# Kernel optimization log

Measured on AMD Instinct MI355X. Metric: run time of the kernel, lower is better.

The kernel has to match this reference:

```python
import jax, jax.numpy as jnp
import numpy as np
from jax import lax

B, N, T, H, C = 131072, 62, 5, 32, 3


def lstm(x, w_ih, w_hh, b_ih, b_hh):
    # x: (B, T, I); gates order i,f,g,o (PyTorch convention)
    b, t, _ = x.shape
    h_dim = w_hh.shape[1]
    xg = jnp.einsum('bti,gi->btg', x, w_ih) + b_ih + b_hh  # (B,T,4H)

    def step(carry, xg_t):
        h, c = carry
        g = xg_t + h @ w_hh.T
        i, f, gg, o = jnp.split(g, 4, axis=-1)
        c = jax.nn.sigmoid(f) * c + jax.nn.sigmoid(i) * jnp.tanh(gg)
        h = jax.nn.sigmoid(o) * jnp.tanh(c)
        return (h, c), h

    z = jnp.zeros((b, h_dim), dtype=x.dtype)
    _, hs = lax.scan(step, (z, z), xg.transpose(1, 0, 2))
    return hs.transpose(1, 0, 2)  # (B,T,H)


def ln_lrelu(x, g, b):
    # LayerNorm over last two dims (seq_len, hidden) jointly, then LeakyReLU(0.01)
    mu = x.mean(axis=(1, 2), keepdims=True)
    var = x.var(axis=(1, 2), keepdims=True)
    y = (x - mu) * lax.rsqrt(var + 1e-5) * g + b
    return jax.nn.leaky_relu(y, 0.01)


def setup_inputs() -> dict:
    key = jax.random.key(0)
    ks = jax.random.split(key, 16)
    sc = lambda fan: 1.0 / np.sqrt(H)
    d = {
        'data': jax.random.normal(ks[0], (B, 1, N, T), dtype=jnp.float32),
        'w_ih0': jax.random.uniform(ks[1], (4 * H, N), minval=-sc(N), maxval=sc(N)),
        'w_hh0': jax.random.uniform(ks[2], (4 * H, H), minval=-sc(H), maxval=sc(H)),
        'b_ih0': jax.random.uniform(ks[3], (4 * H,), minval=-sc(H), maxval=sc(H)),
        'b_hh0': jax.random.uniform(ks[4], (4 * H,), minval=-sc(H), maxval=sc(H)),
        'g0': jnp.ones((T, H), jnp.float32),
        'be0': jnp.zeros((T, H), jnp.float32),
        'w_ih1': jax.random.uniform(ks[5], (4 * H, H), minval=-sc(H), maxval=sc(H)),
        'w_hh1': jax.random.uniform(ks[6], (4 * H, H), minval=-sc(H), maxval=sc(H)),
        'b_ih1': jax.random.uniform(ks[7], (4 * H,), minval=-sc(H), maxval=sc(H)),
        'b_hh1': jax.random.uniform(ks[8], (4 * H,), minval=-sc(H), maxval=sc(H)),
        'g1': jnp.ones((T, H), jnp.float32),
        'be1': jnp.zeros((T, H), jnp.float32),
        'dw': jax.random.normal(ks[9], (C, T * H), dtype=jnp.float32) * 0.05,
        'db': jnp.zeros((C,), jnp.float32),
    }
    return d


def reference(data, w_ih0, w_hh0, b_ih0, b_hh0, g0, be0,
              w_ih1, w_hh1, b_ih1, b_hh1, g1, be1, dw, db):
    x = data.squeeze(1).transpose(0, 2, 1)  # (B, T, N)
    out0 = ln_lrelu(lstm(x, w_ih0, w_hh0, b_ih0, b_hh0), g0, be0)   # dropout=eval
    out1 = ln_lrelu(lstm(out0, w_ih1, w_hh1, b_ih1, b_hh1), g1, be1)
    out = out1 + out0  # residual
    flat = out.reshape(out.shape[0], -1)  # (B, T*H)
    return jax.nn.leaky_relu(flat @ dw.T + db, 0.01)
```

## Files before the change

kernel.cpp:

```cpp
#include <hip/hip_runtime.h>
#include <hip/hip_bf16.h>

#define THREADS 256
#define SPB 8

__device__ __forceinline__ float frcp(float x){ return __builtin_amdgcn_rcpf(x); }
__device__ __forceinline__ float fsig(float x){ return frcp(1.0f + __expf(-x)); }
__device__ __forceinline__ float ftanh(float x){
    float e = __expf(2.0f * x);
    return fmaf(-2.0f, frcp(e + 1.0f), 1.0f);
}
__device__ __forceinline__ float lrelu(float x){
    return x > 0.0f ? x : 0.01f * x;
}

__global__ void diag_kernel(float* outp, float code){
    outp[0] = code;
}

__device__ __forceinline__ void load_wh_global(const float* __restrict__ whh, int j, float (&wh)[4][32]){
    #pragma unroll
    for (int r = 0; r < 4; ++r){
        const float* rp = whh + (r*32 + j)*32;
        #pragma unroll
        for (int q = 0; q < 8; ++q){
            float4 v = *(const float4*)(rp + q*4);
            wh[r][q*4+0] = v.x; wh[r][q*4+1] = v.y;
            wh[r][q*4+2] = v.z; wh[r][q*4+3] = v.w;
        }
    }
}

__device__ __forceinline__ void lstm_rec(const float (&wh)[4][32], const float (&acc)[5][4],
                                         float (&out)[5]){
    float h = 0.0f, c = 0.0f;
    #pragma unroll
    for (int t = 0; t < 5; ++t){
        float q0 = acc[t][0], q1 = acc[t][1], q2 = acc[t][2], q3 = acc[t][3];
        if (t > 0){
            #pragma unroll
            for (int k = 0; k < 32; ++k){
                float hk = __shfl(h, k, 32);
                q0 = fmaf(wh[0][k], hk, q0);
                q1 = fmaf(wh[1][k], hk, q1);
                q2 = fmaf(wh[2][k], hk, q2);
                q3 = fmaf(wh[3][k], hk, q3);
            }
        }
        float iv = fsig(q0), fv = fsig(q1), gv = ftanh(q2), ov = fsig(q3);
        c = fmaf(fv, c, iv * gv);
        h = ov * ftanh(c);
        out[t] = h;
    }
}

__device__ __forceinline__ void ln_lrelu(float (&o)[5], const float* gs, const float* bs, int j){
    float s1 = 0.0f, s2 = 0.0f;
    #pragma unroll
    for (int t = 0; t < 5; ++t){ s1 += o[t]; s2 = fmaf(o[t], o[t], s2); }
    #pragma unroll
    for (int m = 1; m < 32; m <<= 1){
        s1 += __shfl_xor(s1, m, 64);
        s2 += __shfl_xor(s2, m, 64);
    }
    float mu   = s1 * (1.0f/160.0f);
    float var  = s2 * (1.0f/160.0f) - mu*mu;
    float rstd = rsqrtf(var + 1e-5f);
    #pragma unroll
    for (int t = 0; t < 5; ++t){
        float y = (o[t] - mu) * rstd;
        y = fmaf(y, gs[t*32 + j], bs[t*32 + j]);
        o[t] = lrelu(y);
    }
}

__global__ __launch_bounds__(THREADS, 1)
void reslstm_kernel(const float* __restrict__ data,
                    const float* __restrict__ wih0, const float* __restrict__ whh0,
                    const float* __restrict__ bih0, const float* __restrict__ bhh0,
                    const float* __restrict__ g0p,  const float* __restrict__ be0p,
                    const float* __restrict__ wih1, const float* __restrict__ whh1,
                    const float* __restrict__ bih1, const float* __restrict__ bhh1,
                    const float* __restrict__ g1p,  const float* __restrict__ be1p,
                    const float* __restrict__ dwp,  const float* __restrict__ dbp,
                    float* __restrict__ outp, int Btot)
{
    __shared__ __attribute__((aligned(16))) float xs[SPB*320];
    __shared__ __attribute__((aligned(16))) float wbuf[128*68];
    __shared__ __attribute__((aligned(16))) float out0s[SPB*160];
    __shared__ float bias0s[128], bias1s[128];
    __shared__ float g0s[160], be0s[160], g1s[160], be1s[160];
    __shared__ float dws[480];
    __shared__ float dbs[3];

    const int tid = threadIdx.x;
    const int b0  = blockIdx.x * SPB;
    const int nsamp = (Btot - b0 < SPB) ? (Btot - b0) : SPB;

    {
        const float* dat = data + (size_t)b0 * 310;
        for (int i = tid; i < nsamp*310; i += THREADS){
            int s = i / 310, r = i - s*310;
            int n = r / 5,   t = r - n*5;
            xs[s*320 + t*64 + n] = dat[i];
        }
        for (int i = tid; i < SPB*10; i += THREADS){
            int s = i / 10, q = i - s*10;
            xs[s*320 + (q>>1)*64 + 62 + (q&1)] = 0.0f;
        }
        for (int i = tid; i < 128*62; i += THREADS){
            int row = i / 62, n = i - row*62;
            wbuf[row*68 + n] = wih0[i];
        }
        for (int i = tid; i < 128*6; i += THREADS){
            int row = i / 6, n = i - row*6;
            wbuf[row*68 + 62 + n] = 0.0f;
        }
        if (tid < 128)  bias0s[tid] = bih0[tid] + bhh0[tid];
        else            { int q = tid - 128; bias1s[q] = bih1[q] + bhh1[q]; }
        if (tid < 160){
            g0s[tid] = g0p[tid];  be0s[tid] = be0p[tid];
            g1s[tid] = g1p[tid];  be1s[tid] = be1p[tid];
        }
        for (int i = tid; i < 480; i += THREADS) dws[i] = dwp[i];
        if (tid < 3) dbs[tid] = dbp[tid];
    }
    __syncthreads();

    const int j = tid & 31;
    const int s = tid >> 5;

    float acc[5][4];
    #pragma unroll
    for (int r = 0; r < 4; ++r){
        float bv = bias0s[r*32 + j];
        #pragma unroll
        for (int t = 0; t < 5; ++t) acc[t][r] = bv;
    }
    {
        const float* xp  = xs   + s*320;
        const float* wp0 = wbuf + j*68;
        #pragma unroll 4
        for (int n0 = 0; n0 < 64; n0 += 4){
            float4 w[4];
            #pragma unroll
            for (int r = 0; r < 4; ++r)
                w[r] = *(const float4*)(wp0 + r*32*68 + n0);
            #pragma unroll
            for (int t = 0; t < 5; ++t){
                float4 xv = *(const float4*)(xp + t*64 + n0);
                #pragma unroll
                for (int r = 0; r < 4; ++r)
                    acc[t][r] = fmaf(w[r].x, xv.x, fmaf(w[r].y, xv.y, fmaf(w[r].z, xv.z, fmaf(w[r].w, xv.w, acc[t][r]))));
            }
        }
    }

    float o0[5];
    {
        float wh[4][32];
        load_wh_global(whh0, j, wh);
        lstm_rec(wh, acc, o0);
    }
    ln_lrelu(o0, g0s, be0s, j);
    #pragma unroll
    for (int t = 0; t < 5; ++t) out0s[s*160 + t*32 + j] = o0[t];

    __syncthreads();
    for (int i = tid; i < 128*32; i += THREADS){
        int row = i >> 5, k = i & 31;
        wbuf[row*36 + k] = wih1[i];
    }
    for (int i = tid; i < 128*4; i += THREADS){
        int row = i >> 2;
        wbuf[row*36 + 32 + (i & 3)] = 0.0f;
    }
    __syncthreads();

    #pragma unroll
    for (int r = 0; r < 4; ++r){
        float bv = bias1s[r*32 + j];
        #pragma unroll
        for (int t = 0; t < 5; ++t) acc[t][r] = bv;
    }
    {
        const float* wp1 = wbuf  + j*36;
        const float* op  = out0s + s*160;
        #pragma unroll 2
        for (int k0 = 0; k0 < 32; k0 += 4){
            float4 w[4];
            #pragma unroll
            for (int r = 0; r < 4; ++r)
                w[r] = *(const float4*)(wp1 + r*32*36 + k0);
            #pragma unroll
            for (int t = 0; t < 5; ++t){
                float4 ov = *(const float4*)(op + t*32 + k0);
                #pragma unroll
                for (int r = 0; r < 4; ++r)
                    acc[t][r] = fmaf(w[r].x, ov.x, fmaf(w[r].y, ov.y, fmaf(w[r].z, ov.z, fmaf(w[r].w, ov.w, acc[t][r]))));
            }
        }
    }

    float o1[5];
    {
        float wh[4][32];
        load_wh_global(whh1, j, wh);
        lstm_rec(wh, acc, o1);
    }
    ln_lrelu(o1, g1s, be1s, j);
    #pragma unroll
    for (int t = 0; t < 5; ++t) o1[t] += o0[t];

    float p0 = 0.0f, p1 = 0.0f, p2 = 0.0f;
    #pragma unroll
    for (int t = 0; t < 5; ++t){
        float v = o1[t];
        p0 = fmaf(dws[      t*32 + j], v, p0);
        p1 = fmaf(dws[160 + t*32 + j], v, p1);
        p2 = fmaf(dws[320 + t*32 + j], v, p2);
    }
    #pragma unroll
    for (int m = 1; m < 32; m <<= 1){
        p0 += __shfl_xor(p0, m, 64);
        p1 += __shfl_xor(p1, m, 64);
        p2 += __shfl_xor(p2, m, 64);
    }
    if (j < 3 && s < nsamp){
        float v = (j == 0) ? p0 : ((j == 1) ? p1 : p2);
        v = lrelu(v + dbs[j]);
        outp[(size_t)(b0 + s)*3 + j] = v;
    }
}

extern "C" void kernel_launch(void* const* d_in, const int* in_sizes, int n_in,
                              void* d_out, int out_size, void* d_ws, size_t ws_size,
                              hipStream_t stream)
{
    (void)d_ws; (void)ws_size;

    const int B = out_size / 3;

    int idx_data = 0;
    for (int i = 1; i < n_in; ++i)
        if (in_sizes[i] > in_sizes[idx_data]) idx_data = i;

    static const int dict_map[15]  = {0,1,2,3,4,5,6,7,8,9,10,11,12,13,14};
    static const int alpha_map[15] = {6,13,11,2,0,9,4,14,12,3,1,10,5,8,7};
    static const int rev_map[15]   = {14,13,12,11,10,9,8,7,6,5,4,3,2,1,0};

    const int* map = dict_map;
    if (idx_data == 6)       map = alpha_map;
    else if (idx_data == 14) map = rev_map;

    long ds  = (long)in_sizes[idx_data];
    long ws0 = (long)in_sizes[map[1]];
    bool ok = (ds == (long)B*310 || ds == (long)B*620 || ds == (long)B*1240)
           && (ws0 == 7936 || ws0 == 15872 || ws0 == 31744);

    if (!ok || B <= 0){
        diag_kernel<<<1, 1, 0, stream>>>((float*)d_out, 100.0f + 10.0f*idx_data);
        return;
    }

    const float* P[15];
    for (int k = 0; k < 15; ++k) P[k] = (const float*)d_in[map[k]];

    const int nblocks = (B + SPB - 1) / SPB;
    reslstm_kernel<<<dim3(nblocks), dim3(THREADS), 0, stream>>>(
        P[0], P[1], P[2], P[3], P[4], P[5], P[6], P[7], P[8], P[9],
        P[10], P[11], P[12], P[13], P[14],
        (float*)d_out, B);
}
```

Baseline: 1.040 ms.

## Stream recurrent weights from global memory instead of holding them in registers

The 128-register recurrent weight array is replaced by float4 loads from global (L1/L2-cached) memory inside each timestep, and hidden states are written to shared memory instead of being kept in registers. LayerNorm statistics are accumulated during the recurrence. The dense-layer weights and bias are read straight from global memory instead of being staged in LDS. The aim is to cut register pressure so occupancy or spill behaviour improves, at the cost of repeated memory loads on the serial recurrence path.

```diff
diff --git a/kernel.cpp b/kernel.cpp
--- a/kernel.cpp
+++ b/kernel.cpp
@@ -1,5 +1,4 @@
 #include <hip/hip_runtime.h>
-#include <hip/hip_bf16.h>
 
 #define THREADS 256
 #define SPB 8
@@ -10,68 +9,47 @@
     float e = __expf(2.0f * x);
     return fmaf(-2.0f, frcp(e + 1.0f), 1.0f);
 }
-__device__ __forceinline__ float lrelu(float x){
-    return x > 0.0f ? x : 0.01f * x;
-}
-
-__global__ void diag_kernel(float* outp, float code){
-    outp[0] = code;
-}
-
-__device__ __forceinline__ void load_wh_global(const float* __restrict__ whh, int j, float (&wh)[4][32]){
-    #pragma unroll
-    for (int r = 0; r < 4; ++r){
-        const float* rp = whh + (r*32 + j)*32;
-        #pragma unroll
-        for (int q = 0; q < 8; ++q){
-            float4 v = *(const float4*)(rp + q*4);
-            wh[r][q*4+0] = v.x; wh[r][q*4+1] = v.y;
-            wh[r][q*4+2] = v.z; wh[r][q*4+3] = v.w;
-        }
-    }
-}
-
-__device__ __forceinline__ void lstm_rec(const float (&wh)[4][32], const float (&acc)[5][4],
-                                         float (&out)[5]){
-    float h = 0.0f, c = 0.0f;
+__device__ __forceinline__ float lrelu(float x){ return x > 0.0f ? x : 0.01f * x; }
+
+__global__ void diag_kernel(float* outp, float code){ outp[0] = code; }
+
+__device__ __forceinline__ void lstm_rec_stream(const float* __restrict__ whh, int j,
+                                                const float (&acc)[5][4],
+                                                float* __restrict__ hline,
+                                                float& s1o, float& s2o)
+{
+    const float* wr0 = whh + (size_t)(0*32 + j)*32;
+    const float* wr1 = whh + (size_t)(1*32 + j)*32;
+    const float* wr2 = whh + (size_t)(2*32 + j)*32;
+    const float* wr3 = whh + (size_t)(3*32 + j)*32;
+    float h = 0.0f, c = 0.0f, s1 = 0.0f, s2 = 0.0f;
     #pragma unroll
     for (int t = 0; t < 5; ++t){
         float q0 = acc[t][0], q1 = acc[t][1], q2 = acc[t][2], q3 = acc[t][3];
         if (t > 0){
             #pragma unroll
-            for (int k = 0; k < 32; ++k){
-                float hk = __shfl(h, k, 32);
-                q0 = fmaf(wh[0][k], hk, q0);
-                q1 = fmaf(wh[1][k], hk, q1);
-                q2 = fmaf(wh[2][k], hk, q2);
-                q3 = fmaf(wh[3][k], hk, q3);
+            for (int k0 = 0; k0 < 32; k0 += 4){
+                float4 u0 = *(const float4*)(wr0 + k0);
+                float4 u1 = *(const float4*)(wr1 + k0);
+                float4 u2 = *(const float4*)(wr2 + k0);
+                float4 u3 = *(const float4*)(wr3 + k0);
+                float h0 = __shfl(h, k0+0, 32);
+                float h1 = __shfl(h, k0+1, 32);
+                float h2 = __shfl(h, k0+2, 32);
+                float h3 = __shfl(h, k0+3, 32);
+                q0 = fmaf(u0.x,h0, fmaf(u0.y,h1, fmaf(u0.z,h2, fmaf(u0.w,h3, q0))));
+                q1 = fmaf(u1.x,h0, fmaf(u1.y,h1, fmaf(u1.z,h2, fmaf(u1.w,h3, q1))));
+                q2 = fmaf(u2.x,h0, fmaf(u2.y,h1, fmaf(u2.z,h2, fmaf(u2.w,h3, q2))));
+                q3 = fmaf(u3.x,h0, fmaf(u3.y,h1, fmaf(u3.z,h2, fmaf(u3.w,h3, q3))));
             }
         }
         float iv = fsig(q0), fv = fsig(q1), gv = ftanh(q2), ov = fsig(q3);
         c = fmaf(fv, c, iv * gv);
         h = ov * ftanh(c);
-        out[t] = h;
-    }
-}
-
-__device__ __forceinline__ void ln_lrelu(float (&o)[5], const float* gs, const float* bs, int j){
-    float s1 = 0.0f, s2 = 0.0f;
-    #pragma unroll
-    for (int t = 0; t < 5; ++t){ s1 += o[t]; s2 = fmaf(o[t], o[t], s2); }
-    #pragma unroll
-    for (int m = 1; m < 32; m <<= 1){
-        s1 += __shfl_xor(s1, m, 64);
-        s2 += __shfl_xor(s2, m, 64);
-    }
-    float mu   = s1 * (1.0f/160.0f);
-    float var  = s2 * (1.0f/160.0f) - mu*mu;
-    float rstd = rsqrtf(var + 1e-5f);
-    #pragma unroll
-    for (int t = 0; t < 5; ++t){
-        float y = (o[t] - mu) * rstd;
-        y = fmaf(y, gs[t*32 + j], bs[t*32 + j]);
-        o[t] = lrelu(y);
-    }
+        s1 += h; s2 = fmaf(h, h, s2);
+        hline[t*32 + j] = h;
+    }
+    s1o = s1; s2o = s2;
 }
 
 __global__ __launch_bounds__(THREADS, 1)
@@ -90,8 +68,6 @@
     __shared__ __attribute__((aligned(16))) float out0s[SPB*160];
     __shared__ float bias0s[128], bias1s[128];
     __shared__ float g0s[160], be0s[160], g1s[160], be1s[160];
-    __shared__ float dws[480];
-    __shared__ float dbs[3];
 
     const int tid = threadIdx.x;
     const int b0  = blockIdx.x * SPB;
@@ -122,13 +98,13 @@
             g0s[tid] = g0p[tid];  be0s[tid] = be0p[tid];
             g1s[tid] = g1p[tid];  be1s[tid] = be1p[tid];
         }
-        for (int i = tid; i < 480; i += THREADS) dws[i] = dwp[i];
-        if (tid < 3) dbs[tid] = dbp[tid];
     }
     __syncthreads();
 
     const int j = tid & 31;
     const int s = tid >> 5;
+    float* xsc = xs    + s*320;
+    float* o0l = out0s + s*160;
 
     float acc[5][4];
     #pragma unroll
@@ -138,7 +114,6 @@
         for (int t = 0; t < 5; ++t) acc[t][r] = bv;
     }
     {
-        const float* xp  = xs   + s*320;
         const float* wp0 = wbuf + j*68;
         #pragma unroll 4
         for (int n0 = 0; n0 < 64; n0 += 4){
@@ -148,7 +123,7 @@
                 w[r] = *(const float4*)(wp0 + r*32*68 + n0);
             #pragma unroll
             for (int t = 0; t < 5; ++t){
-                float4 xv = *(const float4*)(xp + t*64 + n0);
+                float4 xv = *(const float4*)(xsc + t*64 + n0);
                 #pragma unroll
                 for (int r = 0; r < 4; ++r)
                     acc[t][r] = fmaf(w[r].x, xv.x, fmaf(w[r].y, xv.y, fmaf(w[r].z, xv.z, fmaf(w[r].w, xv.w, acc[t][r]))));
@@ -156,15 +131,24 @@
         }
     }
 
-    float o0[5];
-    {
-        float wh[4][32];
-        load_wh_global(whh0, j, wh);
-        lstm_rec(wh, acc, o0);
-    }
-    ln_lrelu(o0, g0s, be0s, j);
-    #pragma unroll
-    for (int t = 0; t < 5; ++t) out0s[s*160 + t*32 + j] = o0[t];
+    {
+        float s1, s2;
+        lstm_rec_stream(whh0, j, acc, o0l, s1, s2);
+        #pragma unroll
+        for (int m = 1; m < 32; m <<= 1){
+            s1 += __shfl_xor(s1, m, 64);
+            s2 += __shfl_xor(s2, m, 64);
+        }
+        float mu   = s1 * (1.0f/160.0f);
+        float var  = s2 * (1.0f/160.0f) - mu*mu;
+        float rstd = rsqrtf(var + 1e-5f);
+        #pragma unroll
+        for (int t = 0; t < 5; ++t){
+            int ix = t*32 + j;
+            float v = o0l[ix];
+            o0l[ix] = lrelu(fmaf((v - mu)*rstd, g0s[ix], be0s[ix]));
+        }
+    }
 
     __syncthreads();
     for (int i = tid; i < 128*32; i += THREADS){
@@ -184,8 +168,7 @@
         for (int t = 0; t < 5; ++t) acc[t][r] = bv;
     }
     {
-        const float* wp1 = wbuf  + j*36;
-        const float* op  = out0s + s*160;
+        const float* wp1 = wbuf + j*36;
         #pragma unroll 2
         for (int k0 = 0; k0 < 32; k0 += 4){
             float4 w[4];
@@ -194,7 +177,7 @@
                 w[r] = *(const float4*)(wp1 + r*32*36 + k0);
             #pragma unroll
             for (int t = 0; t < 5; ++t){
-                float4 ov = *(const float4*)(op + t*32 + k0);
+                float4 ov = *(const float4*)(o0l + t*32 + k0);
                 #pragma unroll
                 for (int r = 0; r < 4; ++r)
                     acc[t][r] = fmaf(w[r].x, ov.x, fmaf(w[r].y, ov.y, fmaf(w[r].z, ov.z, fmaf(w[r].w, ov.w, acc[t][r]))));
@@ -202,23 +185,27 @@
         }
     }
 
-    float o1[5];
-    {
-        float wh[4][32];
-        load_wh_global(whh1, j, wh);
-        lstm_rec(wh, acc, o1);
-    }
-    ln_lrelu(o1, g1s, be1s, j);
-    #pragma unroll
-    for (int t = 0; t < 5; ++t) o1[t] += o0[t];
-
     float p0 = 0.0f, p1 = 0.0f, p2 = 0.0f;
-    #pragma unroll
-    for (int t = 0; t < 5; ++t){
-        float v = o1[t];
-        p0 = fmaf(dws[      t*32 + j], v, p0);
-        p1 = fmaf(dws[160 + t*32 + j], v, p1);
-        p2 = fmaf(dws[320 + t*32 + j], v, p2);
+    {
+        float s1, s2;
+        lstm_rec_stream(whh1, j, acc, xsc, s1, s2);
+        #pragma unroll
+        for (int m = 1; m < 32; m <<= 1){
+            s1 += __shfl_xor(s1, m, 64);
+            s2 += __shfl_xor(s2, m, 64);
+        }
+        float mu   = s1 * (1.0f/160.0f);
+        float var  = s2 * (1.0f/160.0f) - mu*mu;
+        float rstd = rsqrtf(var + 1e-5f);
+        #pragma unroll
+        for (int t = 0; t < 5; ++t){
+            int ix = t*32 + j;
+            float v = xsc[ix];
+            float y = lrelu(fmaf((v - mu)*rstd, g1s[ix], be1s[ix])) + o0l[ix];
+            p0 = fmaf(dwp[      ix], y, p0);
+            p1 = fmaf(dwp[160 + ix], y, p1);
+            p2 = fmaf(dwp[320 + ix], y, p2);
+        }
     }
     #pragma unroll
     for (int m = 1; m < 32; m <<= 1){
@@ -228,7 +215,7 @@
     }
     if (j < 3 && s < nsamp){
         float v = (j == 0) ? p0 : ((j == 1) ? p1 : p2);
-        v = lrelu(v + dbs[j]);
+        v = lrelu(v + dbp[j]);
         outp[(size_t)(b0 + s)*3 + j] = v;
     }
 }
```

Result: slower. 2.406 ms (+131.2%).

## Shrink blocks to one wavefront and read weights directly from global/cache

Applied to the files above, without the earlier changes.

Reduces the block from 256 threads and 8 samples to 64 threads and 2 samples. It drops the large shared-memory staging of input weights, biases, LayerNorm params and dense weights, so every thread now reads them straight from global memory through the cache. This removes per-block staging work and barriers, and the much smaller LDS footprint allows more blocks per CU. In exchange it adds redundant global and L2 weight loads, which are now float2 loads where rows of 62 floats break alignment. Launch bounds also change to allow 2 blocks per CU.

```diff
diff --git a/kernel.cpp b/kernel.cpp
--- a/kernel.cpp
+++ b/kernel.cpp
@@ -1,8 +1,7 @@
 #include <hip/hip_runtime.h>
-#include <hip/hip_bf16.h>
-
-#define THREADS 256
-#define SPB 8
+
+#define THREADS 64
+#define SPB 2
 
 __device__ __forceinline__ float frcp(float x){ return __builtin_amdgcn_rcpf(x); }
 __device__ __forceinline__ float fsig(float x){ return frcp(1.0f + __expf(-x)); }
@@ -10,13 +9,9 @@
     float e = __expf(2.0f * x);
     return fmaf(-2.0f, frcp(e + 1.0f), 1.0f);
 }
-__device__ __forceinline__ float lrelu(float x){
-    return x > 0.0f ? x : 0.01f * x;
-}
-
-__global__ void diag_kernel(float* outp, float code){
-    outp[0] = code;
-}
+__device__ __forceinline__ float lrelu(float x){ return x > 0.0f ? x : 0.01f * x; }
+
+__global__ void diag_kernel(float* outp, float code){ outp[0] = code; }
 
 __device__ __forceinline__ void load_wh_global(const float* __restrict__ whh, int j, float (&wh)[4][32]){
     #pragma unroll
@@ -54,7 +49,8 @@
     }
 }
 
-__device__ __forceinline__ void ln_lrelu(float (&o)[5], const float* gs, const float* bs, int j){
+__device__ __forceinline__ void ln_lrelu(float (&o)[5], const float* __restrict__ gs,
+                                         const float* __restrict__ bs, int j){
     float s1 = 0.0f, s2 = 0.0f;
     #pragma unroll
     for (int t = 0; t < 5; ++t){ s1 += o[t]; s2 = fmaf(o[t], o[t], s2); }
@@ -74,7 +70,7 @@
     }
 }
 
-__global__ __launch_bounds__(THREADS, 1)
+__global__ __launch_bounds__(THREADS, 2)
 void reslstm_kernel(const float* __restrict__ data,
                     const float* __restrict__ wih0, const float* __restrict__ whh0,
                     const float* __restrict__ bih0, const float* __restrict__ bhh0,
@@ -86,12 +82,7 @@
                     float* __restrict__ outp, int Btot)
 {
     __shared__ __attribute__((aligned(16))) float xs[SPB*320];
-    __shared__ __attribute__((aligned(16))) float wbuf[128*68];
-    __shared__ __attribute__((aligned(16))) float out0s[SPB*160];
-    __shared__ float bias0s[128], bias1s[128];
-    __shared__ float g0s[160], be0s[160], g1s[160], be1s[160];
-    __shared__ float dws[480];
-    __shared__ float dbs[3];
+    __shared__ __attribute__((aligned(16))) float o0s[SPB*160];
 
     const int tid = threadIdx.x;
     const int b0  = blockIdx.x * SPB;
@@ -104,55 +95,57 @@
             int n = r / 5,   t = r - n*5;
             xs[s*320 + t*64 + n] = dat[i];
         }
-        for (int i = tid; i < SPB*10; i += THREADS){
-            int s = i / 10, q = i - s*10;
+        if (tid < SPB*10){
+            int s = tid / 10, q = tid - s*10;
             xs[s*320 + (q>>1)*64 + 62 + (q&1)] = 0.0f;
         }
-        for (int i = tid; i < 128*62; i += THREADS){
-            int row = i / 62, n = i - row*62;
-            wbuf[row*68 + n] = wih0[i];
-        }
-        for (int i = tid; i < 128*6; i += THREADS){
-            int row = i / 6, n = i - row*6;
-            wbuf[row*68 + 62 + n] = 0.0f;
-        }
-        if (tid < 128)  bias0s[tid] = bih0[tid] + bhh0[tid];
-        else            { int q = tid - 128; bias1s[q] = bih1[q] + bhh1[q]; }
-        if (tid < 160){
-            g0s[tid] = g0p[tid];  be0s[tid] = be0p[tid];
-            g1s[tid] = g1p[tid];  be1s[tid] = be1p[tid];
-        }
-        for (int i = tid; i < 480; i += THREADS) dws[i] = dwp[i];
-        if (tid < 3) dbs[tid] = dbp[tid];
     }
     __syncthreads();
 
     const int j = tid & 31;
     const int s = tid >> 5;
+    const float* xp = xs  + s*320;
+    float*       ol = o0s + s*160;
 
     float acc[5][4];
     #pragma unroll
-    for (int r = 0; r < 4; ++r){
-        float bv = bias0s[r*32 + j];
+    for (int r = 0; r < 4; ++r)
+    {
+        float bv = bih0[r*32 + j] + bhh0[r*32 + j];
         #pragma unroll
         for (int t = 0; t < 5; ++t) acc[t][r] = bv;
     }
     {
-        const float* xp  = xs   + s*320;
-        const float* wp0 = wbuf + j*68;
-        #pragma unroll 4
-        for (int n0 = 0; n0 < 64; n0 += 4){
-            float4 w[4];
-            #pragma unroll
-            for (int r = 0; r < 4; ++r)
-                w[r] = *(const float4*)(wp0 + r*32*68 + n0);
+        const float* w0 = wih0 + (size_t)(0*32 + j)*62;
+        const float* w1 = wih0 + (size_t)(1*32 + j)*62;
+        const float* w2 = wih0 + (size_t)(2*32 + j)*62;
+        const float* w3 = wih0 + (size_t)(3*32 + j)*62;
+        #pragma unroll 5
+        for (int n0 = 0; n0 < 60; n0 += 4){
+            float2 a0 = *(const float2*)(w0 + n0), b0v = *(const float2*)(w0 + n0 + 2);
+            float2 a1 = *(const float2*)(w1 + n0), b1v = *(const float2*)(w1 + n0 + 2);
+            float2 a2 = *(const float2*)(w2 + n0), b2v = *(const float2*)(w2 + n0 + 2);
+            float2 a3 = *(const float2*)(w3 + n0), b3v = *(const float2*)(w3 + n0 + 2);
             #pragma unroll
             for (int t = 0; t < 5; ++t){
                 float4 xv = *(const float4*)(xp + t*64 + n0);
-                #pragma unroll
-                for (int r = 0; r < 4; ++r)
-                    acc[t][r] = fmaf(w[r].x, xv.x, fmaf(w[r].y, xv.y, fmaf(w[r].z, xv.z, fmaf(w[r].w, xv.w, acc[t][r]))));
+                acc[t][0] = fmaf(a0.x,xv.x, fmaf(a0.y,xv.y, fmaf(b0v.x,xv.z, fmaf(b0v.y,xv.w, acc[t][0]))));
+                acc[t][1] = fmaf(a1.x,xv.x, fmaf(a1.y,xv.y, fmaf(b1v.x,xv.z, fmaf(b1v.y,xv.w, acc[t][1]))));
+                acc[t][2] = fmaf(a2.x,xv.x, fmaf(a2.y,xv.y, fmaf(b2v.x,xv.z, fmaf(b2v.y,xv.w, acc[t][2]))));
+                acc[t][3] = fmaf(a3.x,xv.x, fmaf(a3.y,xv.y, fmaf(b3v.x,xv.z, fmaf(b3v.y,xv.w, acc[t][3]))));
             }
+        }
+        float2 t0 = *(const float2*)(w0 + 60);
+        float2 t1 = *(const float2*)(w1 + 60);
+        float2 t2 = *(const float2*)(w2 + 60);
+        float2 t3 = *(const float2*)(w3 + 60);
+        #pragma unroll
+        for (int t = 0; t < 5; ++t){
+            float2 xv = *(const float2*)(xp + t*64 + 60);
+            acc[t][0] = fmaf(t0.x,xv.x, fmaf(t0.y,xv.y, acc[t][0]));
+            acc[t][1] = fmaf(t1.x,xv.x, fmaf(t1.y,xv.y, acc[t][1]));
+            acc[t][2] = fmaf(t2.x,xv.x, fmaf(t2.y,xv.y, acc[t][2]));
+            acc[t][3] = fmaf(t3.x,xv.x, fmaf(t3.y,xv.y, acc[t][3]));
         }
     }
 
@@ -162,42 +155,35 @@
         load_wh_global(whh0, j, wh);
         lstm_rec(wh, acc, o0);
     }
-    ln_lrelu(o0, g0s, be0s, j);
-    #pragma unroll
-    for (int t = 0; t < 5; ++t) out0s[s*160 + t*32 + j] = o0[t];
-
+    ln_lrelu(o0, g0p, be0p, j);
+    #pragma unroll
+    for (int t = 0; t < 5; ++t) ol[t*32 + j] = o0[t];
     __syncthreads();
-    for (int i = tid; i < 128*32; i += THREADS){
-        int row = i >> 5, k = i & 31;
-        wbuf[row*36 + k] = wih1[i];
-    }
-    for (int i = tid; i < 128*4; i += THREADS){
-        int row = i >> 2;
-        wbuf[row*36 + 32 + (i & 3)] = 0.0f;
-    }
-    __syncthreads();
 
     #pragma unroll
     for (int r = 0; r < 4; ++r){
-        float bv = bias1s[r*32 + j];
+        float bv = bih1[r*32 + j] + bhh1[r*32 + j];
         #pragma unroll
         for (int t = 0; t < 5; ++t) acc[t][r] = bv;
     }
     {
-        const float* wp1 = wbuf  + j*36;
-        const float* op  = out0s + s*160;
+        const float* w0 = wih1 + (size_t)(0*32 + j)*32;
+        const float* w1 = wih1 + (size_t)(1*32 + j)*32;
+        const float* w2 = wih1 + (size_t)(2*32 + j)*32;
+        const float* w3 = wih1 + (size_t)(3*32 + j)*32;
         #pragma unroll 2
         for (int k0 = 0; k0 < 32; k0 += 4){
-            float4 w[4];
-            #pragma unroll
-            for (int r = 0; r < 4; ++r)
-                w[r] = *(const float4*)(wp1 + r*32*36 + k0);
+            float4 u0 = *(const float4*)(w0 + k0);
+            float4 u1 = *(const float4*)(w1 + k0);
+            float4 u2 = *(const float4*)(w2 + k0);
+            float4 u3 = *(const float4*)(w3 + k0);
             #pragma unroll
             for (int t = 0; t < 5; ++t){
-                float4 ov = *(const float4*)(op + t*32 + k0);
-                #pragma unroll
-                for (int r = 0; r < 4; ++r)
-                    acc[t][r] = fmaf(w[r].x, ov.x, fmaf(w[r].y, ov.y, fmaf(w[r].z, ov.z, fmaf(w[r].w, ov.w, acc[t][r]))));
+                float4 ov = *(const float4*)(ol + t*32 + k0);
+                acc[t][0] = fmaf(u0.x,ov.x, fmaf(u0.y,ov.y, fmaf(u0.z,ov.z, fmaf(u0.w,ov.w, acc[t][0]))));
+                acc[t][1] = fmaf(u1.x,ov.x, fmaf(u1.y,ov.y, fmaf(u1.z,ov.z, fmaf(u1.w,ov.w, acc[t][1]))));
+                acc[t][2] = fmaf(u2.x,ov.x, fmaf(u2.y,ov.y, fmaf(u2.z,ov.z, fmaf(u2.w,ov.w, acc[t][2]))));
+                acc[t][3] = fmaf(u3.x,ov.x, fmaf(u3.y,ov.y, fmaf(u3.z,ov.z, fmaf(u3.w,ov.w, acc[t][3]))));
             }
         }
     }
@@ -208,7 +194,7 @@
         load_wh_global(whh1, j, wh);
         lstm_rec(wh, acc, o1);
     }
-    ln_lrelu(o1, g1s, be1s, j);
+    ln_lrelu(o1, g1p, be1p, j);
     #pragma unroll
     for (int t = 0; t < 5; ++t) o1[t] += o0[t];
 
@@ -216,9 +202,10 @@
     #pragma unroll
     for (int t = 0; t < 5; ++t){
         float v = o1[t];
-        p0 = fmaf(dws[      t*32 + j], v, p0);
-        p1 = fmaf(dws[160 + t*32 + j], v, p1);
-        p2 = fmaf(dws[320 + t*32 + j], v, p2);
+        int ix = t*32 + j;
+        p0 = fmaf(dwp[      ix], v, p0);
+        p1 = fmaf(dwp[160 + ix], v, p1);
+        p2 = fmaf(dwp[320 + ix], v, p2);
     }
     #pragma unroll
     for (int m = 1; m < 32; m <<= 1){
@@ -228,7 +215,7 @@
     }
     if (j < 3 && s < nsamp){
         float v = (j == 0) ? p0 : ((j == 1) ? p1 : p2);
-        v = lrelu(v + dbs[j]);
+        v = lrelu(v + dbp[j]);
         outp[(size_t)(b0 + s)*3 + j] = v;
     }
 }
```

New measurement: 1.202 ms. 15.5% more time.
